# Performance work log

Hardware: AMD Instinct MI355X
Metric: run time of the kernel (lower is better)

The kernel has to match this reference:

```python
import heapq
import jax, jax.numpy as jnp
import numpy as np

NB_CLASSES = 50257
INPUT_DIM = 512
BATCH = 1024
NB_REQ = 8


def build_huffman(nb_classes):
    """Replicates Huffmax.build: huffman tree over equal frequencies,
    codes padded with 0, paths padded with root node id."""
    heap = [(1, i, i) for i in range(nb_classes)]  # (freq, tiebreak, payload)
    heapq.heapify(heap)
    node_id = 0
    tiebreak = nb_classes
    while len(heap) > 1:
        f1, _, left = heapq.heappop(heap)
        f2, _, right = heapq.heappop(heap)
        heapq.heappush(heap, (f1 + f2, tiebreak, ('n', node_id, left, right)))
        node_id += 1
        tiebreak += 1
    root = heap[0][2]
    total_nodes = node_id  # = nb_classes - 1
    root_id = root[1]
    codes, paths = {}, {}
    stack = [(root, [], [])]
    while stack:
        node, code, path = stack.pop()
        if isinstance(node, tuple):
            _, nid, l, r = node
            stack.append((l, code + [0], path + [nid]))
            stack.append((r, code + [1], path + [nid]))
        else:
            codes[node] = code
            paths[node] = path
    max_depth = max(len(c) for c in codes.values())
    code_arr = np.zeros((nb_classes, max_depth), np.float32)
    path_arr = np.full((nb_classes, max_depth), root_id, np.int32)
    for c in range(nb_classes):
        code_arr[c, :len(codes[c])] = codes[c]
        path_arr[c, :len(paths[c])] = paths[c]
    return code_arr, path_arr, total_nodes


def setup_inputs() -> dict:
    key = jax.random.key(0)
    k1, k2, k3 = jax.random.split(key, 3)
    code_arr, path_arr, total_nodes = build_huffman(NB_CLASSES)
    input_vector = jax.random.normal(k1, (BATCH, INPUT_DIM), dtype=jnp.float32)
    target_classes = jax.random.randint(k2, (BATCH, NB_REQ), 0, NB_CLASSES, dtype=jnp.int32)
    # glorot-ish scaled node weights (original W is (total_nodes, input_dim, 1))
    W = jax.random.normal(k3, (total_nodes, INPUT_DIM), dtype=jnp.float32) * (1.0 / np.sqrt(INPUT_DIM))
    b = jnp.zeros((total_nodes,), dtype=jnp.float32)
    return {
        'input_vector': input_vector,
        'target_classes': target_classes,
        'W': W,
        'b': b,
        'class_paths': jnp.asarray(path_arr),
        'huffman_codes': jnp.asarray(code_arr),
    }


def reference(input_vector, target_classes, W, b, class_paths, huffman_codes):
    # req_nodes: (B, R, D) node ids along huffman path for each requested class
    req_nodes = class_paths[target_classes]
    # req_W: (B, R, D, I) gathered node weight rows; y = x . W_node + b_node
    req_W = W[req_nodes]
    y = jnp.einsum('bi,brdi->brd', input_vector, req_W) + b[req_nodes]
    y = jax.nn.sigmoid(y)
    codes = huffman_codes[target_classes]  # (B, R, D) in {0,1} (0-padded)
    # factor = y if code==0 else (1-y); product along the path
    return jnp.prod(codes + y - 2.0 * codes * y, axis=-1)
```

## Files before the change

kernel.cpp:

```cpp
#include <hip/hip_runtime.h>
#include <hip/hip_bf16.h>
#include <math.h>

#define WAVES_PER_BLOCK 4

__global__ __launch_bounds__(WAVES_PER_BLOCK * 64)
void huffmax_kernel(const float* __restrict__ x,
                    const int*   __restrict__ tgt,
                    const float* __restrict__ W,
                    const float* __restrict__ bias,
                    const int*   __restrict__ paths,
                    const float* __restrict__ codes,
                    float*       __restrict__ out,
                    int B, int R, int D, int I)
{
    const int lane = threadIdx.x & 63;
    const int wave = threadIdx.x >> 6;
    const int p = blockIdx.x * WAVES_PER_BLOCK + wave;
    if (p >= B * R) return;
    const int b = p / R;

    const float4* xrow = reinterpret_cast<const float4*>(x + (size_t)b * I);
    const float4 x0 = xrow[lane * 2 + 0];
    const float4 x1 = xrow[lane * 2 + 1];

    const int c = tgt[p];
    const int*   path = paths + (size_t)c * D;
    const float* code = codes + (size_t)c * D;

    float prod = 1.0f;
    for (int d = 0; d < D; ++d) {
        const int node = path[d];
        const float4* wrow = reinterpret_cast<const float4*>(W + (size_t)node * I);
        const float4 w0 = wrow[lane * 2 + 0];
        const float4 w1 = wrow[lane * 2 + 1];
        float acc = x0.x * w0.x + x0.y * w0.y + x0.z * w0.z + x0.w * w0.w
                  + x1.x * w1.x + x1.y * w1.y + x1.z * w1.z + x1.w * w1.w;
        #pragma unroll
        for (int off = 32; off; off >>= 1)
            acc += __shfl_xor(acc, off, 64);
        const float t = acc + bias[node];
        const float y = 1.0f / (1.0f + expf(-t));
        const float cd = code[d];
        prod *= cd + y - 2.0f * cd * y;
    }
    if (lane == 0) out[p] = prod;
}

extern "C" void kernel_launch(void* const* d_in, const int* in_sizes, int n_in,
                              void* d_out, int out_size, void* d_ws, size_t ws_size,
                              hipStream_t stream) {
    const float* x     = (const float*)d_in[0];
    const int*   tgt   = (const int*)  d_in[1];
    const float* W     = (const float*)d_in[2];
    const float* bias  = (const float*)d_in[3];
    const int*   paths = (const int*)  d_in[4];
    const float* codes = (const float*)d_in[5];
    float* out = (float*)d_out;

    const int N = in_sizes[3];
    const int C = N + 1;
    const int I = in_sizes[2] / N;
    const int B = in_sizes[0] / I;
    const int R = in_sizes[1] / B;
    const int D = in_sizes[4] / C;

    const int pairs = B * R;
    const int grid = (pairs + WAVES_PER_BLOCK - 1) / WAVES_PER_BLOCK;
    huffmax_kernel<<<grid, WAVES_PER_BLOCK * 64, 0, stream>>>(
        x, tgt, W, bias, paths, codes, out, B, R, D, I);
}
```

Baseline: 28.32 us.

## Template on path depth, issue all node-row loads before batched reductions

Specializes the kernel on the Huffman depth D so that every gathered weight-row load for a path is issued up front into a register array. The per-level cross-lane reductions are then done together, interleaved across levels, instead of one serialized load-reduce-sigmoid chain per level. Path ids, codes and biases are loaded once per lane and broadcast by shuffle. The sigmoid/code product is rewritten as 1/prod(1+exp(-s*t)) using fast __expf, and x/W loads use lane-contiguous float4 indexing for coalescing. This trades higher register use for more memory-level parallelism, and the fast exp may slightly change accuracy.

Result: faster. 25.45 us (-10.1%).

```diff
diff --git a/kernel.cpp b/kernel.cpp
--- a/kernel.cpp
+++ b/kernel.cpp
@@ -1,50 +1,93 @@
 #include <hip/hip_runtime.h>
-#include <hip/hip_bf16.h>
 #include <math.h>
 
-#define WAVES_PER_BLOCK 4
+#define WPB 4
 
-__global__ __launch_bounds__(WAVES_PER_BLOCK * 64)
-void huffmax_kernel(const float* __restrict__ x,
-                    const int*   __restrict__ tgt,
-                    const float* __restrict__ W,
-                    const float* __restrict__ bias,
-                    const int*   __restrict__ paths,
-                    const float* __restrict__ codes,
-                    float*       __restrict__ out,
-                    int B, int R, int D, int I)
+template<int D>
+__global__ __launch_bounds__(WPB * 64, 4)
+void huff_kernel(const float* __restrict__ x,
+                 const int*   __restrict__ tgt,
+                 const float* __restrict__ W,
+                 const float* __restrict__ bias,
+                 const int*   __restrict__ paths,
+                 const float* __restrict__ codes,
+                 float*       __restrict__ out,
+                 int R, int I, int npairs)
 {
     const int lane = threadIdx.x & 63;
-    const int wave = threadIdx.x >> 6;
-    const int p = blockIdx.x * WAVES_PER_BLOCK + wave;
-    if (p >= B * R) return;
+    const int wv   = threadIdx.x >> 6;
+    const int p    = blockIdx.x * WPB + wv;
+    if (p >= npairs) return;
     const int b = p / R;
 
     const float4* xrow = reinterpret_cast<const float4*>(x + (size_t)b * I);
-    const float4 x0 = xrow[lane * 2 + 0];
-    const float4 x1 = xrow[lane * 2 + 1];
+    const float4 xa = xrow[lane];
+    const float4 xb = xrow[lane + 64];
 
+    const int c  = tgt[p];
+    const int dd = (lane < D) ? lane : (D - 1);
+    const int   nd = paths[(size_t)c * D + dd];
+    const float cd = codes[(size_t)c * D + dd];
+    const float bv = bias[nd];
+    const float sd = 1.0f - 2.0f * cd;
+
+    float acc[D];
+    #pragma unroll
+    for (int d = 0; d < D; ++d) {
+        const int node = __shfl(nd, d, 64);
+        const float4* wr = reinterpret_cast<const float4*>(W + (size_t)node * I);
+        const float4 wa = wr[lane];
+        const float4 wb = wr[lane + 64];
+        acc[d] = xa.x * wa.x + xa.y * wa.y + xa.z * wa.z + xa.w * wa.w
+               + xb.x * wb.x + xb.y * wb.y + xb.z * wb.z + xb.w * wb.w;
+    }
+
+    #pragma unroll
+    for (int off = 32; off; off >>= 1) {
+        #pragma unroll
+        for (int d = 0; d < D; ++d)
+            acc[d] += __shfl_xor(acc[d], off, 64);
+    }
+
+    float q = 1.0f;
+    #pragma unroll
+    for (int d = 0; d < D; ++d) {
+        const float t = acc[d] + __shfl(bv, d, 64);
+        const float s = __shfl(sd, d, 64);
+        q *= 1.0f + __expf(-s * t);
+    }
+    if (lane == 0) out[p] = 1.0f / q;
+}
+
+__global__ __launch_bounds__(WPB * 64)
+void huff_kernel_gen(const float* __restrict__ x, const int* __restrict__ tgt,
+                     const float* __restrict__ W, const float* __restrict__ bias,
+                     const int* __restrict__ paths, const float* __restrict__ codes,
+                     float* __restrict__ out, int R, int I, int D, int npairs)
+{
+    const int lane = threadIdx.x & 63;
+    const int p = blockIdx.x * WPB + (threadIdx.x >> 6);
+    if (p >= npairs) return;
+    const int b = p / R;
+    const float4* xrow = reinterpret_cast<const float4*>(x + (size_t)b * I);
+    const float4 xa = xrow[lane];
+    const float4 xb = xrow[lane + 64];
     const int c = tgt[p];
-    const int*   path = paths + (size_t)c * D;
-    const float* code = codes + (size_t)c * D;
-
-    float prod = 1.0f;
+    float q = 1.0f;
     for (int d = 0; d < D; ++d) {
-        const int node = path[d];
-        const float4* wrow = reinterpret_cast<const float4*>(W + (size_t)node * I);
-        const float4 w0 = wrow[lane * 2 + 0];
-        const float4 w1 = wrow[lane * 2 + 1];
-        float acc = x0.x * w0.x + x0.y * w0.y + x0.z * w0.z + x0.w * w0.w
-                  + x1.x * w1.x + x1.y * w1.y + x1.z * w1.z + x1.w * w1.w;
+        const int node = paths[(size_t)c * D + d];
+        const float4* wr = reinterpret_cast<const float4*>(W + (size_t)node * I);
+        const float4 wa = wr[lane];
+        const float4 wb = wr[lane + 64];
+        float acc = xa.x * wa.x + xa.y * wa.y + xa.z * wa.z + xa.w * wa.w
+                  + xb.x * wb.x + xb.y * wb.y + xb.z * wb.z + xb.w * wb.w;
         #pragma unroll
-        for (int off = 32; off; off >>= 1)
-            acc += __shfl_xor(acc, off, 64);
+        for (int off = 32; off; off >>= 1) acc += __shfl_xor(acc, off, 64);
         const float t = acc + bias[node];
-        const float y = 1.0f / (1.0f + expf(-t));
-        const float cd = code[d];
-        prod *= cd + y - 2.0f * cd * y;
+        const float s = 1.0f - 2.0f * codes[(size_t)c * D + d];
+        q *= 1.0f + __expf(-s * t);
     }
-    if (lane == 0) out[p] = prod;
+    if (lane == 0) out[p] = 1.0f / q;
 }
 
 extern "C" void kernel_launch(void* const* d_in, const int* in_sizes, int n_in,
@@ -65,8 +108,14 @@
     const int R = in_sizes[1] / B;
     const int D = in_sizes[4] / C;
 
-    const int pairs = B * R;
-    const int grid = (pairs + WAVES_PER_BLOCK - 1) / WAVES_PER_BLOCK;
-    huffmax_kernel<<<grid, WAVES_PER_BLOCK * 64, 0, stream>>>(
-        x, tgt, W, bias, paths, codes, out, B, R, D, I);
+    const int npairs = B * R;
+    const int grid = (npairs + WPB - 1) / WPB;
+
+    switch (D) {
+    case 15: huff_kernel<15><<<grid, WPB * 64, 0, stream>>>(x, tgt, W, bias, paths, codes, out, R, I, npairs); break;
+    case 16: huff_kernel<16><<<grid, WPB * 64, 0, stream>>>(x, tgt, W, bias, paths, codes, out, R, I, npairs); break;
+    case 17: huff_kernel<17><<<grid, WPB * 64, 0, stream>>>(x, tgt, W, bias, paths, codes, out, R, I, npairs); break;
+    case 18: huff_kernel<18><<<grid, WPB * 64, 0, stream>>>(x, tgt, W, bias, paths, codes, out, R, I, npairs); break;
+    default: huff_kernel_gen<<<grid, WPB * 64, 0, stream>>>(x, tgt, W, bias, paths, codes, out, R, I, D, npairs); break;
+    }
 }
```
